# Performance work log

Measured on AMD Instinct MI355X. Metric: run time of the kernel, lower is better.

Reference implementation:

```python
import jax, jax.numpy as jnp
import numpy as np

B, C, T, H, W, L = 4, 256, 8, 16, 16, 8
NO = 8                # num_offsets
D = C // NO           # per-head feature dim for offset/weight MLPs
EPS = 1e-5


def setup_inputs() -> dict:
    key = jax.random.key(0)
    ks = jax.random.split(key, 6)
    return {
        "features": jax.random.normal(ks[0], (B, C, T, H, W, L), jnp.float32),
        "pos": jax.random.normal(ks[1], (B, C, T, H, W, L), jnp.float32),
        "Wp": jax.random.normal(ks[2], (C, 3 * C), jnp.float32) * 0.02,  # 1x1x1 conv: 3C -> C
        "bp": jnp.zeros((C,), jnp.float32),
        "Wo": jax.random.normal(ks[3], (D, 3), jnp.float32) * 0.02,      # offset_embed Linear(d,3)
        "bo": jnp.zeros((3,), jnp.float32),
        "Ww": jax.random.normal(ks[4], (D, 2), jnp.float32) * 0.02,      # weight_embed Linear(d,2)
        "bw": jnp.zeros((2,), jnp.float32),
    }


def _trilinear_sample(feat, coords):
    """feat: (N,C,D1,D2,D3); coords: (N,G,3) in [-1,1] (axis order D1,D2,D3).
    align_corners=False, zeros padding (matches F.grid_sample semantics)."""
    N, Cc, D1, D2, D3 = feat.shape
    sizes = jnp.asarray([D1, D2, D3], feat.dtype)
    pix = ((coords + 1.0) * sizes - 1.0) * 0.5       # unnormalize to pixel coords
    lo = jnp.floor(pix)
    frac = pix - lo                                   # (N,G,3)
    lo = lo.astype(jnp.int32)
    dims = jnp.asarray([D1, D2, D3], jnp.int32)
    feat_flat = feat.reshape(N, Cc, D1 * D2 * D3)
    out = jnp.zeros((N, Cc, coords.shape[1]), feat.dtype)
    for dz in (0, 1):
        for dy in (0, 1):
            for dx in (0, 1):
                off = jnp.asarray([dz, dy, dx], jnp.int32)
                idx = lo + off                        # (N,G,3)
                wz = jnp.where(dz, frac[..., 0], 1.0 - frac[..., 0])
                wy = jnp.where(dy, frac[..., 1], 1.0 - frac[..., 1])
                wx = jnp.where(dx, frac[..., 2], 1.0 - frac[..., 2])
                wgt = wz * wy * wx                    # (N,G)
                valid = jnp.all((idx >= 0) & (idx < dims), axis=-1)
                idc = jnp.clip(idx, 0, dims - 1)
                lin = (idc[..., 0] * D2 + idc[..., 1]) * D3 + idc[..., 2]  # (N,G)
                vals = jnp.take_along_axis(feat_flat, lin[:, None, :], axis=2)  # (N,C,G)
                out = out + vals * (wgt * valid)[:, None, :]
    return out


def reference(features, pos, Wp, bp, Wo, bo, Ww, bw):
    Bv, Cv, Tv, Hv, Wv, Lv = features.shape
    BT = Bv * Tv
    feat = features.transpose(0, 2, 1, 3, 4, 5).reshape(BT, Cv, Hv, Wv, Lv)
    posr = pos.transpose(0, 2, 1, 3, 4, 5).reshape(BT, Cv, Hv, Wv, Lv)
    # global context + projection (1x1x1 conv over 3C channels) + ReLU
    glob = feat.mean(axis=(2, 3, 4), keepdims=True)
    src = jnp.concatenate([feat, posr, jnp.broadcast_to(glob, feat.shape)], axis=1)  # (BT,3C,H,W,L)
    proj = jax.nn.relu(jnp.einsum('nixyz,oi->noxyz', src, Wp) + bp[None, :, None, None, None])
    osrc = proj.transpose(0, 2, 3, 4, 1).reshape(BT, Hv, Wv, Lv, NO, D)
    # per-voxel per-head offsets in (0,1) and scalar weights
    offset = jax.nn.sigmoid(osrc @ Wo + bo)                      # (BT,H,W,L,NO,3)
    wgt = jax.nn.softmax(osrc @ Ww + bw, axis=-1)[..., 1]        # (BT,H,W,L,NO)
    # base flow field in [-1,1], deform in logit space, re-sigmoid
    base = jnp.stack(jnp.meshgrid(jnp.linspace(-1.0, 1.0, Hv),
                                  jnp.linspace(-1.0, 1.0, Wv),
                                  jnp.linspace(-1.0, 1.0, Lv), indexing='ij'), axis=-1)
    base01 = jnp.clip((base + 1.0) * 0.5, EPS, 1.0 - EPS)
    logit = jnp.log(base01 / (1.0 - base01))                     # (H,W,L,3)
    sp = jax.nn.sigmoid(logit[None, :, :, :, None, :] + offset)  # (BT,H,W,L,NO,3)
    grid = (sp * 2.0 - 1.0).transpose(0, 4, 1, 2, 3, 5).reshape(BT, NO * Hv * Wv * Lv, 3)
    sampled = _trilinear_sample(feat, grid).reshape(BT, Cv, NO, Hv, Wv, Lv)
    out = feat + jnp.einsum('bcnhwl,bhwln->bchwl', sampled, wgt)
    return out.reshape(Bv, Tv, Cv, Hv, Wv, Lv).transpose(0, 2, 1, 3, 4, 5)
```

## Files before the change

### kernel.cpp

```cpp
#include <hip/hip_runtime.h>

#define BB 4
#define CC 256
#define TT 8
#define HH 16
#define WW 16
#define LL 8
#define NO 8
#define DD 32
#define BT 32
#define VV 2048
#define KIN 512
#define EPS_ 1e-5f

typedef short bf16x8 __attribute__((ext_vector_type(8)));
typedef float f32x4 __attribute__((ext_vector_type(4)));
typedef float f32x2 __attribute__((ext_vector_type(2)));

static __device__ __forceinline__ float b2f(unsigned short u) {
    return __uint_as_float(((unsigned int)u) << 16);
}
static __device__ __forceinline__ float b2f_lo(unsigned int x) {
    return __uint_as_float(x << 16);
}
static __device__ __forceinline__ float b2f_hi(unsigned int x) {
    return __uint_as_float(x & 0xffff0000u);
}
static __device__ __forceinline__ unsigned short f2b(float f) {
    unsigned int x = __float_as_uint(f);
    unsigned int r = x + 0x7fffu + ((x >> 16) & 1u);
    return (unsigned short)(r >> 16);
}
static __device__ __forceinline__ unsigned int f2b_pk(float lo, float hi) {
    return (unsigned int)f2b(lo) | ((unsigned int)f2b(hi) << 16);
}
static __device__ __forceinline__ float sigm(float x) {
    return 1.0f / (1.0f + __expf(-x));
}

__global__ __launch_bounds__(256) void k0_prep(const float* __restrict__ Wp,
                                               unsigned short* __restrict__ Wa) {
    int i = blockIdx.x * 256 + threadIdx.x;
    int o = i >> 9, k = i & 511;
    Wa[i] = f2b(Wp[o * 768 + k]);
}

__global__ __launch_bounds__(256) void k1_transpose(const float* __restrict__ features,
                                                    const float* __restrict__ pos,
                                                    unsigned short* __restrict__ srcT) {
    const int vt = blockIdx.x;
    const int ch = blockIdx.y;
    const int n  = blockIdx.z;
    const int v0 = vt * 32;
    const int b = n >> 3, t = n & 7;
    const int tid = threadIdx.x;
    const int wv = tid >> 6;
    const int lane = tid & 63;
    const int cg = lane >> 3;
    const int vg = lane & 7;

    __shared__ unsigned short sf[32 * 130];
    __shared__ unsigned short sp[32 * 130];

    const int lcbase = wv * 8 + cg;
    const size_t base = (((size_t)b * CC + ch * 128) * TT + t) * (size_t)VV + v0 + vg * 4;
    float4 fv[4], pv[4];
    #pragma unroll
    for (int it = 0; it < 4; ++it) {
        const size_t idx = base + (size_t)(lcbase + it * 32) * (TT * VV);
        fv[it] = *(const float4*)(features + idx);
        pv[it] = *(const float4*)(pos + idx);
    }
    #pragma unroll
    for (int it = 0; it < 4; ++it) {
        const int lc = lcbase + it * 32;
        const int vb = vg * 4;
        sf[(vb + 0) * 130 + lc] = f2b(fv[it].x);
        sf[(vb + 1) * 130 + lc] = f2b(fv[it].y);
        sf[(vb + 2) * 130 + lc] = f2b(fv[it].z);
        sf[(vb + 3) * 130 + lc] = f2b(fv[it].w);
        sp[(vb + 0) * 130 + lc] = f2b(pv[it].x);
        sp[(vb + 1) * 130 + lc] = f2b(pv[it].y);
        sp[(vb + 2) * 130 + lc] = f2b(pv[it].z);
        sp[(vb + 3) * 130 + lc] = f2b(pv[it].w);
    }
    __syncthreads();

    unsigned int* srcU = (unsigned int*)srcT;
    const int vi = tid >> 7;
    const int j  = tid & 127;
    const int kuint = (j < 64) ? (ch * 64 + j) : (128 + ch * 64 + (j - 64));
    const int lj2 = (j < 64) ? (2 * j) : (2 * (j - 64));
    const unsigned short* lsrc = (j < 64) ? sf : sp;
    const size_t obase = ((size_t)n * VV + v0) * 256 + kuint;
    #pragma unroll 8
    for (int vp = 0; vp < 32; vp += 2) {
        const int v = vp + vi;
        srcU[obase + (size_t)v * 256] = *(const unsigned int*)&lsrc[v * 130 + lj2];
    }
}

__global__ __launch_bounds__(256) void k2a_gsum(const unsigned short* __restrict__ srcT,
                                                float* __restrict__ gpart) {
    const int n = blockIdx.x;
    const int vs = blockIdx.y;
    const int tid = threadIdx.x;
    const int ku = tid & 127;
    const int vh = tid >> 7;
    const unsigned int* srcU = (const unsigned int*)srcT;
    const size_t base = ((size_t)n * VV + vs * 128 + vh * 64) * 256 + ku;
    float sl = 0.f, sh = 0.f;
    #pragma unroll 8
    for (int i = 0; i < 64; ++i) {
        unsigned int u = srcU[base + (size_t)i * 256];
        sl += b2f_lo(u);
        sh += b2f_hi(u);
    }
    float2* gp = (float2*)gpart;
    gp[((size_t)n * 32 + vs * 2 + vh) * 128 + ku] = make_float2(sl, sh);
}

__global__ __launch_bounds__(256) void k2_gterm(const float* __restrict__ gpart,
                                                const float* __restrict__ Wp,
                                                const float* __restrict__ bp,
                                                float* __restrict__ gterm) {
    const int n = blockIdx.x;
    const int o = threadIdx.x;
    __shared__ float gl[CC];
    float s = 0.0f;
    const float* gp = gpart + (size_t)n * 32 * CC + o;
    #pragma unroll 8
    for (int vt = 0; vt < 32; ++vt) s += gp[vt * CC];
    gl[o] = s * (1.0f / (float)VV);
    __syncthreads();
    const float4* wrow = (const float4*)(Wp + (size_t)o * 768 + 512);
    const float4* g4 = (const float4*)gl;
    float acc = bp[o];
    #pragma unroll 8
    for (int c = 0; c < 64; ++c) {
        float4 w = wrow[c], g = g4[c];
        acc += w.x * g.x + w.y * g.y + w.z * g.z + w.w * g.w;
    }
    gterm[n * CC + o] = acc;
}

__global__ __launch_bounds__(256) void k3_gemm(const unsigned short* __restrict__ Wa,
                                               const unsigned short* __restrict__ srcT,
                                               const float* __restrict__ gterm,
                                               unsigned short* __restrict__ projT) {
    const int n  = blockIdx.x;
    const int mb = blockIdx.y;
    const int nb = blockIdx.z;
    const int tid = threadIdx.x;
    const int m0 = mb * 128, v0 = nb * 128;

    __shared__ short As[128 * 40];
    __shared__ short Bs[128 * 40];

    const int wv = tid >> 6;
    const int lane = tid & 63;
    const int wm = wv >> 1, wn = wv & 1;
    const int lr = lane & 15, lq = lane >> 4;

    f32x4 acc[4][4];
    #pragma unroll
    for (int i = 0; i < 4; ++i)
        #pragma unroll
        for (int j = 0; j < 4; ++j)
            acc[i][j] = (f32x4){0.f, 0.f, 0.f, 0.f};

    const int row = tid >> 1, half = tid & 1;
    const unsigned short* agp = Wa + (size_t)(m0 + row) * KIN + half * 16;
    const unsigned short* bgp = srcT + ((size_t)n * VV + v0 + row) * KIN + half * 16;
    short* asp = &As[row * 40 + half * 16];
    short* bsp = &Bs[row * 40 + half * 16];

    for (int k0 = 0; k0 < KIN; k0 += 32) {
        uint4 a0 = *(const uint4*)(agp + k0);
        uint4 a1 = *(const uint4*)(agp + k0 + 8);
        uint4 b0 = *(const uint4*)(bgp + k0);
        uint4 b1 = *(const uint4*)(bgp + k0 + 8);
        __syncthreads();
        *(uint4*)asp = a0; *(uint4*)(asp + 8) = a1;
        *(uint4*)bsp = b0; *(uint4*)(bsp + 8) = b1;
        __syncthreads();

        bf16x8 af[4], bf[4];
        #pragma unroll
        for (int i = 0; i < 4; ++i)
            af[i] = *(const bf16x8*)&As[(wm * 64 + i * 16 + lr) * 40 + lq * 8];
        #pragma unroll
        for (int j = 0; j < 4; ++j)
            bf[j] = *(const bf16x8*)&Bs[(wn * 64 + j * 16 + lr) * 40 + lq * 8];
        #pragma unroll
        for (int i = 0; i < 4; ++i)
            #pragma unroll
            for (int j = 0; j < 4; ++j)
                acc[i][j] = __builtin_amdgcn_mfma_f32_16x16x32_bf16(af[i], bf[j], acc[i][j], 0, 0, 0);
    }

    #pragma unroll
    for (int i = 0; i < 4; ++i) {
        const int og = m0 + wm * 64 + i * 16 + lq * 4;
        float4 g = *(const float4*)(gterm + n * CC + og);
        #pragma unroll
        for (int j = 0; j < 4; ++j) {
            const int vg = v0 + wn * 64 + j * 16 + lr;
            float x0 = fmaxf(acc[i][j][0] + g.x, 0.0f);
            float x1 = fmaxf(acc[i][j][1] + g.y, 0.0f);
            float x2 = fmaxf(acc[i][j][2] + g.z, 0.0f);
            float x3 = fmaxf(acc[i][j][3] + g.w, 0.0f);
            ushort4 st;
            st.x = f2b(x0); st.y = f2b(x1); st.z = f2b(x2); st.w = f2b(x3);
            *(ushort4*)&projT[((size_t)n * VV + vg) * CC + og] = st;
        }
    }
}

__global__ __launch_bounds__(256) void k4_coef(const unsigned short* __restrict__ projT,
                                               const float* __restrict__ Wo,
                                               const float* __restrict__ bo,
                                               const float* __restrict__ Ww,
                                               const float* __restrict__ bw,
                                               int2* __restrict__ pairs) {
    __shared__ float sWo[96], sWw[64], sb[5];
    const int tid = threadIdx.x;
    if (tid < 96) sWo[tid] = Wo[tid];
    if (tid < 64) sWw[tid] = Ww[tid];
    if (tid < 3)  sb[tid] = bo[tid];
    if (tid < 2)  sb[3 + tid] = bw[tid];
    __syncthreads();

    const int g = blockIdx.x * 256 + tid;
    const int n = g >> 14;
    const int rem = g & 16383;
    const int v = rem >> 3;
    const int hd = rem & 7;

    const uint4* up = (const uint4*)(projT + ((size_t)n * VV + v) * CC + hd * DD);
    float osrc[32];
    #pragma unroll
    for (int q = 0; q < 4; ++q) {
        uint4 u = up[q];
        unsigned int ws4[4] = {u.x, u.y, u.z, u.w};
        #pragma unroll
        for (int e = 0; e < 4; ++e) {
            osrc[q * 8 + e * 2]     = b2f_lo(ws4[e]);
            osrc[q * 8 + e * 2 + 1] = b2f_hi(ws4[e]);
        }
    }

    float o0 = sb[0], o1 = sb[1], o2 = sb[2];
    float zw = sb[4] - sb[3];
    #pragma unroll
    for (int d = 0; d < DD; ++d) {
        float t = osrc[d];
        o0 += t * sWo[3 * d + 0];
        o1 += t * sWo[3 * d + 1];
        o2 += t * sWo[3 * d + 2];
        zw += t * (sWw[2 * d + 1] - sWw[2 * d]);
    }
    const float wgt = sigm(zw);

    const int h = v >> 7, w = (v >> 3) & 15, l = v & 7;
    float ph = fminf(fmaxf(h * (1.0f / 15.0f), EPS_), 1.0f - EPS_);
    float pw = fminf(fmaxf(w * (1.0f / 15.0f), EPS_), 1.0f - EPS_);
    float pl = fminf(fmaxf(l * (1.0f / 7.0f),  EPS_), 1.0f - EPS_);
    float lh = __logf(ph / (1.0f - ph));
    float lw = __logf(pw / (1.0f - pw));
    float ll = __logf(pl / (1.0f - pl));

    float sph = sigm(lh + sigm(o0));
    float spw = sigm(lw + sigm(o1));
    float spl = sigm(ll + sigm(o2));
    float pixh = sph * 16.0f - 0.5f;
    float pixw = spw * 16.0f - 0.5f;
    float pixl = spl * 8.0f  - 0.5f;

    float flh = floorf(pixh), flw = floorf(pixw), fll = floorf(pixl);
    float fh = pixh - flh, fw = pixw - flw, fl = pixl - fll;
    int ih = (int)flh, iw = (int)flw, il = (int)fll;

    int2* pp = pairs + (size_t)g * 8;
    #pragma unroll
    for (int dz = 0; dz < 2; ++dz)
        #pragma unroll
        for (int dy = 0; dy < 2; ++dy)
            #pragma unroll
            for (int dx = 0; dx < 2; ++dx) {
                int iz = ih + dz, iy = iw + dy, ix = il + dx;
                float wt = (dz ? fh : 1.0f - fh) * (dy ? fw : 1.0f - fw) * (dx ? fl : 1.0f - fl) * wgt;
                bool valid = ((unsigned)iz < 16u) && ((unsigned)iy < 16u) && ((unsigned)ix < 8u);
                int lin = valid ? (((iz * 16 + iy) * 8 + ix) << 10) : 0;
                float wv2 = valid ? wt : 0.0f;
                pp[dz * 4 + dy * 2 + dx] = make_int2(lin, __float_as_int(wv2));
            }
}

__global__ __launch_bounds__(256) void k5_gather(const unsigned short* __restrict__ srcT,
                                                 const int2* __restrict__ pairs,
                                                 unsigned short* __restrict__ res) {
    __shared__ int   sK[4 * 64];
    __shared__ float sW[4 * 64];
    const int tid = threadIdx.x;
    const int wid = tid >> 6;
    const int lane = tid & 63;
    const int gv = blockIdx.x * 4 + wid;
    const int n = gv >> 11;
    const int v = gv & 2047;

    int2 q = pairs[(size_t)gv * 64 + lane];
    int key = q.x;
    float w = __int_as_float(q.y);

    #pragma unroll
    for (int k = 2; k <= 64; k <<= 1) {
        #pragma unroll
        for (int j = k >> 1; j > 0; j >>= 1) {
            int pk = __shfl_xor(key, j);
            float pw = __shfl_xor(w, j);
            bool keepMin = (((lane & k) == 0) == ((lane & j) == 0));
            bool take = keepMin ? (pk < key) : (pk > key);
            if (take) { key = pk; w = pw; }
        }
    }
    #pragma unroll
    for (int d = 1; d < 64; d <<= 1) {
        float tw = __shfl_up(w, d);
        int   tk = __shfl_up(key, d);
        if (lane >= d && tk == key) w += tw;
    }
    int nk = __shfl_down(key, 1);
    bool tail = (lane == 63) || (nk != key);
    unsigned long long mask = __ballot(tail);
    int cnt = __popcll(mask);
    int cidx = __popcll(mask & ((1ull << lane) - 1ull));

    sK[wid * 64 + lane] = 0;
    sW[wid * 64 + lane] = 0.0f;
    __syncthreads();
    if (tail) { sK[wid * 64 + cidx] = key; sW[wid * 64 + cidx] = w; }
    __syncthreads();
    int ck = sK[wid * 64 + lane];
    float cw = sW[wid * 64 + lane];

    const char* slabB = (const char*)srcT + (size_t)n * VV * KIN * 2 + lane * 8;
    float a0 = 0.f, a1 = 0.f, a2 = 0.f, a3 = 0.f;
    const int iters = (cnt + 7) & ~7;
    #pragma unroll 1
    for (int e = 0; e < iters; e += 8) {
        uint2 f[8]; float wv[8];
        #pragma unroll
        for (int u = 0; u < 8; ++u) {
            int rk = __shfl(ck, e + u);
            wv[u] = __shfl(cw, e + u);
            f[u] = *(const uint2*)(slabB + (unsigned)rk);
        }
        #pragma unroll
        for (int u = 0; u < 8; ++u) {
            a0 = fmaf(wv[u], b2f_lo(f[u].x), a0);
            a1 = fmaf(wv[u], b2f_hi(f[u].x), a1);
            a2 = fmaf(wv[u], b2f_lo(f[u].y), a2);
            a3 = fmaf(wv[u], b2f_hi(f[u].y), a3);
        }
    }

    uint2 st;
    st.x = f2b_pk(a0, a1);
    st.y = f2b_pk(a2, a3);
    *(uint2*)&res[((size_t)n * VV + v) * CC + lane * 4] = st;
}

__global__ __launch_bounds__(256) void k6_final(const float* __restrict__ features,
                                                const unsigned short* __restrict__ res,
                                                float* __restrict__ out) {
    const int n = blockIdx.x;
    const int c0 = blockIdx.y * 64;
    const int v0 = blockIdx.z * 64;
    const int b = n >> 3, t = n & 7;
    const int tid = threadIdx.x;
    const int ty = tid >> 6, tx = tid & 63;

    __shared__ unsigned short t6[64 * 66];

    for (int vv = ty; vv < 64; vv += 4)
        t6[vv * 66 + tx] = res[((size_t)n * VV + v0 + vv) * CC + c0 + tx];
    __syncthreads();
    for (int cc = ty; cc < 64; cc += 4) {
        int c = c0 + cc;
        size_t oidx = (((size_t)b * CC + c) * TT + t) * VV + v0 + tx;
        out[oidx] = features[oidx] + b2f(t6[tx * 66 + cc]);
    }
}

extern "C" void kernel_launch(void* const* d_in, const int* in_sizes, int n_in,
                              void* d_out, int out_size, void* d_ws, size_t ws_size,
                              hipStream_t stream) {
    (void)in_sizes; (void)n_in; (void)out_size; (void)ws_size;
    const float* features = (const float*)d_in[0];
    const float* pos      = (const float*)d_in[1];
    const float* Wp       = (const float*)d_in[2];
    const float* bp       = (const float*)d_in[3];
    const float* Wo       = (const float*)d_in[4];
    const float* bo       = (const float*)d_in[5];
    const float* Ww       = (const float*)d_in[6];
    const float* bw       = (const float*)d_in[7];
    float* out = (float*)d_out;

    char* ws = (char*)d_ws;
    unsigned short* srcT  = (unsigned short*)ws;
    unsigned short* Wa    = (unsigned short*)(ws + 67108864);
    float*          gterm = (float*)(ws + 67403776);
    unsigned short* projT = (unsigned short*)(ws + 67436544);
    int2*           pairs = (int2*)(ws + 100990976);
    float*          gpart = (float*)(ws + 100990976);
    unsigned short* res   = projT;

    k0_prep<<<512, 256, 0, stream>>>(Wp, Wa);
    k1_transpose<<<dim3(64, 2, 32), 256, 0, stream>>>(features, pos, srcT);
    k2a_gsum<<<dim3(32, 16), 256, 0, stream>>>(srcT, gpart);
    k2_gterm<<<32, 256, 0, stream>>>(gpart, Wp, bp, gterm);
    k3_gemm<<<dim3(32, 2, 16), 256, 0, stream>>>(Wa, srcT, gterm, projT);
    k4_coef<<<2048, 256, 0, stream>>>(projT, Wo, bo, Ww, bw, pairs);
    k5_gather<<<16384, 256, 0, stream>>>(srcT, pairs, res);
    k6_final<<<dim3(32, 4, 32), 256, 0, stream>>>(features, res, out);
}
```

Baseline: 343.9 us.

## Fuse global-sum into transpose kernel and use direct-to-LDS loads in GEMM

The transpose kernel now also computes the per-channel global partial sums with warp shuffles, so the separate k2a_gsum pass that re-read srcT is removed. The transpose itself is restructured: each block handles one array over 64 voxels, stages fp32 in LDS, and writes 16-byte packed bf16 rows. The GEMM switches its global-to-LDS staging to global_load_lds with an unpadded 32-wide LDS layout, which avoids register round-trips but may add LDS bank conflicts on the fragment reads. The gsum is now computed from fp32 before bf16 rounding, which changes numerics slightly.

```diff
diff --git a/kernel.cpp b/kernel.cpp
--- a/kernel.cpp
+++ b/kernel.cpp
@@ -15,7 +15,6 @@
 
 typedef short bf16x8 __attribute__((ext_vector_type(8)));
 typedef float f32x4 __attribute__((ext_vector_type(4)));
-typedef float f32x2 __attribute__((ext_vector_type(2)));
 
 static __device__ __forceinline__ float b2f(unsigned short u) {
     return __uint_as_float(((unsigned int)u) << 16);
@@ -36,6 +35,11 @@
 }
 static __device__ __forceinline__ float sigm(float x) {
     return 1.0f / (1.0f + __expf(-x));
+}
+static __device__ __forceinline__ void glds16(const void* g, void* l) {
+    __builtin_amdgcn_global_load_lds(
+        (const __attribute__((address_space(1))) void*)g,
+        (__attribute__((address_space(3))) void*)l, 16, 0, 0);
 }
 
 __global__ __launch_bounds__(256) void k0_prep(const float* __restrict__ Wp,
@@ -47,77 +51,73 @@
 
 __global__ __launch_bounds__(256) void k1_transpose(const float* __restrict__ features,
                                                     const float* __restrict__ pos,
-                                                    unsigned short* __restrict__ srcT) {
-    const int vt = blockIdx.x;
-    const int ch = blockIdx.y;
-    const int n  = blockIdx.z;
-    const int v0 = vt * 32;
+                                                    unsigned short* __restrict__ srcT,
+                                                    float* __restrict__ gpart) {
+    const int vt  = blockIdx.x;
+    const int ch  = blockIdx.y & 1;
+    const int arr = blockIdx.y >> 1;
+    const int n   = blockIdx.z;
+    const int v0 = vt * 64;
     const int b = n >> 3, t = n & 7;
     const int tid = threadIdx.x;
-    const int wv = tid >> 6;
+    const int w = tid >> 6;
     const int lane = tid & 63;
-    const int cg = lane >> 3;
-    const int vg = lane & 7;
-
-    __shared__ unsigned short sf[32 * 130];
-    __shared__ unsigned short sp[32 * 130];
-
-    const int lcbase = wv * 8 + cg;
-    const size_t base = (((size_t)b * CC + ch * 128) * TT + t) * (size_t)VV + v0 + vg * 4;
-    float4 fv[4], pv[4];
-    #pragma unroll
-    for (int it = 0; it < 4; ++it) {
-        const size_t idx = base + (size_t)(lcbase + it * 32) * (TT * VV);
-        fv[it] = *(const float4*)(features + idx);
-        pv[it] = *(const float4*)(pos + idx);
-    }
-    #pragma unroll
-    for (int it = 0; it < 4; ++it) {
-        const int lc = lcbase + it * 32;
-        const int vb = vg * 4;
-        sf[(vb + 0) * 130 + lc] = f2b(fv[it].x);
-        sf[(vb + 1) * 130 + lc] = f2b(fv[it].y);
-        sf[(vb + 2) * 130 + lc] = f2b(fv[it].z);
-        sf[(vb + 3) * 130 + lc] = f2b(fv[it].w);
-        sp[(vb + 0) * 130 + lc] = f2b(pv[it].x);
-        sp[(vb + 1) * 130 + lc] = f2b(pv[it].y);
-        sp[(vb + 2) * 130 + lc] = f2b(pv[it].z);
-        sp[(vb + 3) * 130 + lc] = f2b(pv[it].w);
-    }
-    __syncthreads();
-
-    unsigned int* srcU = (unsigned int*)srcT;
-    const int vi = tid >> 7;
-    const int j  = tid & 127;
-    const int kuint = (j < 64) ? (ch * 64 + j) : (128 + ch * 64 + (j - 64));
-    const int lj2 = (j < 64) ? (2 * j) : (2 * (j - 64));
-    const unsigned short* lsrc = (j < 64) ? sf : sp;
-    const size_t obase = ((size_t)n * VV + v0) * 256 + kuint;
-    #pragma unroll 8
-    for (int vp = 0; vp < 32; vp += 2) {
-        const int v = vp + vi;
-        srcU[obase + (size_t)v * 256] = *(const unsigned int*)&lsrc[v * 130 + lj2];
-    }
-}
-
-__global__ __launch_bounds__(256) void k2a_gsum(const unsigned short* __restrict__ srcT,
-                                                float* __restrict__ gpart) {
-    const int n = blockIdx.x;
-    const int vs = blockIdx.y;
-    const int tid = threadIdx.x;
-    const int ku = tid & 127;
-    const int vh = tid >> 7;
-    const unsigned int* srcU = (const unsigned int*)srcT;
-    const size_t base = ((size_t)n * VV + vs * 128 + vh * 64) * 256 + ku;
-    float sl = 0.f, sh = 0.f;
-    #pragma unroll 8
-    for (int i = 0; i < 64; ++i) {
-        unsigned int u = srcU[base + (size_t)i * 256];
-        sl += b2f_lo(u);
-        sh += b2f_hi(u);
-    }
-    float2* gp = (float2*)gpart;
-    gp[((size_t)n * 32 + vs * 2 + vh) * 128 + ku] = make_float2(sl, sh);
+    const int cs  = lane >> 4;
+    const int v16 = lane & 15;
+
+    __shared__ float s1[64 * 132];
+
+    const float* src = arr ? pos : features;
+    const float* bp0 = src + ((size_t)(b * CC + ch * 128 + w * 32 + cs) * TT + t) * (size_t)VV
+                           + v0 + v16 * 4;
+
+    float4 fv[8];
+    #pragma unroll
+    for (int i = 0; i < 8; ++i)
+        fv[i] = *(const float4*)(bp0 + (size_t)i * 4 * TT * VV);
+
+    float part[8];
+    #pragma unroll
+    for (int i = 0; i < 8; ++i) {
+        const int c_l = w * 32 + i * 4 + cs;
+        float* dst = &s1[(v16 * 4) * 132 + c_l];
+        dst[0 * 132] = fv[i].x;
+        dst[1 * 132] = fv[i].y;
+        dst[2 * 132] = fv[i].z;
+        dst[3 * 132] = fv[i].w;
+        part[i] = fv[i].x + fv[i].y + fv[i].z + fv[i].w;
+    }
+
+    if (arr == 0) {
+        #pragma unroll
+        for (int i = 0; i < 8; ++i) {
+            #pragma unroll
+            for (int m = 1; m < 16; m <<= 1)
+                part[i] += __shfl_xor(part[i], m);
+        }
+        if (v16 == 0) {
+            #pragma unroll
+            for (int i = 0; i < 8; ++i)
+                gpart[((size_t)n * 32 + vt) * CC + ch * 128 + w * 32 + i * 4 + cs] = part[i];
+        }
+    }
+    __syncthreads();
+
+    const int vo = tid >> 2, q = tid & 3;
+    const float* row = &s1[vo * 132];
+    unsigned short* ob = srcT + ((size_t)n * VV + v0 + vo) * KIN + arr * 256 + ch * 128;
+    #pragma unroll
+    for (int j = 0; j < 4; ++j) {
+        const int c0 = j * 32 + q * 8;
+        float4 f0 = *(const float4*)(row + c0);
+        float4 f1 = *(const float4*)(row + c0 + 4);
+        uint4 o;
+        o.x = f2b_pk(f0.x, f0.y);
+        o.y = f2b_pk(f0.z, f0.w);
+        o.z = f2b_pk(f1.x, f1.y);
+        o.w = f2b_pk(f1.z, f1.w);
+        *(uint4*)(ob + c0) = o;
+    }
 }
 
 __global__ __launch_bounds__(256) void k2_gterm(const float* __restrict__ gpart,
@@ -154,12 +154,12 @@
     const int tid = threadIdx.x;
     const int m0 = mb * 128, v0 = nb * 128;
 
-    __shared__ short As[128 * 40];
-    __shared__ short Bs[128 * 40];
-
-    const int wv = tid >> 6;
+    __shared__ short As[128 * 32];
+    __shared__ short Bs[128 * 32];
+
+    const int w = tid >> 6;
     const int lane = tid & 63;
-    const int wm = wv >> 1, wn = wv & 1;
+    const int wm = w >> 1, wn = w & 1;
     const int lr = lane & 15, lq = lane >> 4;
 
     f32x4 acc[4][4];
@@ -169,29 +169,30 @@
         for (int j = 0; j < 4; ++j)
             acc[i][j] = (f32x4){0.f, 0.f, 0.f, 0.f};
 
-    const int row = tid >> 1, half = tid & 1;
-    const unsigned short* agp = Wa + (size_t)(m0 + row) * KIN + half * 16;
-    const unsigned short* bgp = srcT + ((size_t)n * VV + v0 + row) * KIN + half * 16;
-    short* asp = &As[row * 40 + half * 16];
-    short* bsp = &Bs[row * 40 + half * 16];
+    const int rsub = lane >> 2;
+    const int ksub = (lane & 3) * 8;
+    const unsigned short* agp = Wa   + (size_t)(m0 + w * 16 + rsub) * KIN + ksub;
+    const unsigned short* bgp = srcT + ((size_t)n * VV + v0 + w * 16 + rsub) * KIN + ksub;
+    short* alds0 = &As[(w * 16) * 32];
+    short* alds1 = &As[(64 + w * 16) * 32];
+    short* blds0 = &Bs[(w * 16) * 32];
+    short* blds1 = &Bs[(64 + w * 16) * 32];
 
     for (int k0 = 0; k0 < KIN; k0 += 32) {
-        uint4 a0 = *(const uint4*)(agp + k0);
-        uint4 a1 = *(const uint4*)(agp + k0 + 8);
-        uint4 b0 = *(const uint4*)(bgp + k0);
-        uint4 b1 = *(const uint4*)(bgp + k0 + 8);
         __syncthreads();
-        *(uint4*)asp = a0; *(uint4*)(asp + 8) = a1;
-        *(uint4*)bsp = b0; *(uint4*)(bsp + 8) = b1;
+        glds16(agp + k0,                   alds0);
+        glds16(agp + k0 + (size_t)64 * KIN, alds1);
+        glds16(bgp + k0,                   blds0);
+        glds16(bgp + k0 + (size_t)64 * KIN, blds1);
         __syncthreads();
 
         bf16x8 af[4], bf[4];
         #pragma unroll
         for (int i = 0; i < 4; ++i)
-            af[i] = *(const bf16x8*)&As[(wm * 64 + i * 16 + lr) * 40 + lq * 8];
+            af[i] = *(const bf16x8*)&As[(wm * 64 + i * 16 + lr) * 32 + lq * 8];
         #pragma unroll
         for (int j = 0; j < 4; ++j)
-            bf[j] = *(const bf16x8*)&Bs[(wn * 64 + j * 16 + lr) * 40 + lq * 8];
+            bf[j] = *(const bf16x8*)&Bs[(wn * 64 + j * 16 + lr) * 32 + lq * 8];
         #pragma unroll
         for (int i = 0; i < 4; ++i)
             #pragma unroll
@@ -417,8 +418,7 @@
     unsigned short* res   = projT;
 
     k0_prep<<<512, 256, 0, stream>>>(Wp, Wa);
-    k1_transpose<<<dim3(64, 2, 32), 256, 0, stream>>>(features, pos, srcT);
-    k2a_gsum<<<dim3(32, 16), 256, 0, stream>>>(srcT, gpart);
+    k1_transpose<<<dim3(32, 4, 32), 256, 0, stream>>>(features, pos, srcT, gpart);
     k2_gterm<<<32, 256, 0, stream>>>(gpart, Wp, bp, gterm);
     k3_gemm<<<dim3(32, 2, 16), 256, 0, stream>>>(Wa, srcT, gterm, projT);
     k4_coef<<<2048, 256, 0, stream>>>(projT, Wo, bo, Ww, bw, pairs);
```

Result: faster. 330.5 us (-3.9%).
